# Performance work log

Hardware: AMD Instinct MI355X
Metric: run time of the kernel (lower is better)

Reference implementation:

```python
import jax, jax.numpy as jnp
import numpy as np

B, N, D = 2, 2048, 1024
H, FD, HD = 16, 16, 64
ENC = 512
EPS = 1e-12
RD = 4.0            # sqrt(scale_dim=feature_dim=16)
RRD = 2.0           # sqrt(RD)
R2 = float(np.sqrt(2.0))


def taylor_exp(x):
    # x: [..., fd] -> [..., 1 + fd + fd*fd]
    x2 = (x[..., :, None] * x[..., None, :]).reshape(*x.shape[:-1], FD * FD) / R2
    return jnp.concatenate([jnp.ones_like(x[..., :1]), x / RRD, x2 / RD], axis=-1)


def setup_inputs() -> dict:
    key = jax.random.key(0)
    ks = jax.random.split(key, 7)
    s = 1.0 / np.sqrt(D)
    x = jax.random.normal(ks[0], (B, N, D), dtype=jnp.float32)
    Wq = jax.random.normal(ks[1], (H * FD, D), dtype=jnp.float32) * s
    Wk = jax.random.normal(ks[2], (H * FD, D), dtype=jnp.float32) * s
    Wv = jax.random.normal(ks[3], (H * HD, D), dtype=jnp.float32) * s
    Wk_enc = jax.random.normal(ks[4], (H * FD, D), dtype=jnp.float32) * s
    Wv_enc = jax.random.normal(ks[5], (H * HD, D), dtype=jnp.float32) * s
    Wout = jax.random.normal(ks[6], (D, H * HD), dtype=jnp.float32) * s
    return {"x": x, "Wq": Wq, "Wk": Wk, "Wv": Wv,
            "Wk_enc": Wk_enc, "Wv_enc": Wv_enc, "Wout": Wout}


def reference(x, Wq, Wk, Wv, Wk_enc, Wv_enc, Wout):
    b, n, _ = x.shape
    # projections -> [b, h, n, *]
    q = (x @ Wq.T).reshape(b, n, H, FD).transpose(0, 2, 1, 3)
    k = (x @ Wk.T).reshape(b, n, H, FD).transpose(0, 2, 1, 3)
    v = (x @ Wv.T).reshape(b, n, H, HD).transpose(0, 2, 1, 3)
    # encoder prefix
    x_enc = x[:, :ENC]
    k_enc = (x_enc @ Wk_enc.T).reshape(b, ENC, H, FD).transpose(0, 2, 1, 3)
    v_enc = (x_enc @ Wv_enc.T).reshape(b, ENC, H, HD).transpose(0, 2, 1, 3)
    # Taylor feature maps: fd -> 1 + fd + fd^2 = 273
    k_enc_f = taylor_exp(k_enc)
    q_f = taylor_exp(q)
    k_f = taylor_exp(k)
    # causal decoder attention (unnormalized)
    A_qk = jnp.einsum('bhnd,bhmd->bhnm', q_f, k_f)
    A_qk = jnp.tril(A_qk)
    y1 = jnp.einsum('bhnm,bhme->bhne', A_qk, v)
    # cross attention to encoder prefix
    A_qk2 = jnp.einsum('bhnd,bhmd->bhnm', q_f, k_enc_f)
    y2 = jnp.einsum('bhnm,bhme->bhne', A_qk2, v_enc)
    # shared normalizer: enc sum + causal cumsum of decoder key features
    k_state = k_enc_f.sum(axis=2, keepdims=True) + jnp.cumsum(k_f, axis=2)
    z = 1.0 / ((q_f * k_state).sum(axis=-1) + EPS)  # [b, h, n]
    out = (y1 + y2) * z[..., None]                  # [b, h, n, hd]
    out = out.transpose(0, 2, 1, 3).reshape(b, n, H * HD)
    return out @ Wout.T
```

## Files before the change

kernel.cpp:

```cpp
#include <hip/hip_runtime.h>

#define B_    2
#define N_    2048
#define H_    16
#define HD_   64
#define ENC_  512
#define FP_   288
#define CHK_  64
#define NC_   32
#define SSZ_  18720
#define C2C_  0.17677669529663687f
#define EPS_  1e-12f

using s8v   = __attribute__((ext_vector_type(8))) short;
using s4v   = __attribute__((ext_vector_type(4))) short;
using h8v   = __attribute__((ext_vector_type(8))) _Float16;
using f4v   = __attribute__((ext_vector_type(4))) float;
using u16x4 = __attribute__((ext_vector_type(4))) unsigned short;
typedef unsigned short ushort_t;

__device__ __forceinline__ unsigned short f16q(float x) {
    _Float16 h = (_Float16)x;
    return __builtin_bit_cast(unsigned short, h);
}
__device__ __forceinline__ float f16f(unsigned short u) {
    return (float)__builtin_bit_cast(_Float16, u);
}
__device__ __forceinline__ u16x4 f16q4(float4 v) {
    return (u16x4){f16q(v.x), f16q(v.y), f16q(v.z), f16q(v.w)};
}

#define MFMAH_ __builtin_amdgcn_mfma_f32_16x16x32_f16

__device__ __forceinline__ void gld16(const void* g, void* l) {
    __builtin_amdgcn_global_load_lds(
        (const __attribute__((address_space(1))) unsigned int*)g,
        (__attribute__((address_space(3))) unsigned int*)l, 16, 0, 0);
}

__device__ __forceinline__ int xcd_swz(int b, int nwg) {
    int q = nwg >> 3, r = nwg & 7;
    int xcd = b & 7, loc = b >> 3;
    return (xcd < r ? xcd * (q + 1) : r * (q + 1) + (xcd - r) * q) + loc;
}

#define X_F4   1048576
#define W1_F4  393216
#define W2_F4  327680
#define WO_F4  262144

__global__ __launch_bounds__(256) void split_all(
    const float* __restrict__ x,
    const float* __restrict__ Wq, const float* __restrict__ Wk,
    const float* __restrict__ Wv, const float* __restrict__ Wke,
    const float* __restrict__ Wve, const float* __restrict__ Wout,
    ushort_t* __restrict__ xh,
    ushort_t* __restrict__ w1, ushort_t* __restrict__ w2,
    ushort_t* __restrict__ wo)
{
    int gid = blockIdx.x * 256 + threadIdx.x;
    if (gid < X_F4) {
        ((u16x4*)xh)[gid] = f16q4(((const float4*)x)[gid]);
    } else if (gid < X_F4 + W1_F4) {
        int i = gid - X_F4;
        int row = i >> 8, c4 = i & 255;
        const float* s = (row < 256) ? Wq + (size_t)row * 1024
                       : (row < 512) ? Wk + (size_t)(row - 256) * 1024
                                     : Wv + (size_t)(row - 512) * 1024;
        ((u16x4*)w1)[i] = f16q4(*(const float4*)(s + c4 * 4));
    } else if (gid < X_F4 + W1_F4 + W2_F4) {
        int i = gid - X_F4 - W1_F4;
        int row = i >> 8, c4 = i & 255;
        const float* s = (row < 256) ? Wke + (size_t)row * 1024
                                     : Wve + (size_t)(row - 256) * 1024;
        ((u16x4*)w2)[i] = f16q4(*(const float4*)(s + c4 * 4));
    } else {
        int i = gid - X_F4 - W1_F4 - W2_F4;
        ((u16x4*)wo)[i] = f16q4(((const float4*)Wout)[i]);
    }
}

template <int SHIFT>
__device__ __forceinline__ void bg128(
    const ushort_t* __restrict__ Ah, const ushort_t* __restrict__ Wh,
    int bx, int by, int rowjump,
    ushort_t* SM, f4v (&acc)[4][4])
{
    int t = threadIdx.x;
    int w = t >> 6, lane = t & 63;
    int row0 = by * 128, col0 = bx * 128;
    int wrow = (w >> 1) * 64, wcol = (w & 1) * 64;
    int fr = lane & 15, g = lane >> 4;

    int c0 = lane, c1 = 64 + lane;
    int r0 = w * 32 + (c0 >> 2), k80 = (c0 & 3) * 8;
    int r1 = w * 32 + (c1 >> 2), k81 = (c1 & 3) * 8;
    int gr0 = row0 + r0, gr1 = row0 + r1;
    size_t a0 = (size_t)(gr0 >> SHIFT) * rowjump + (gr0 & ((1 << SHIFT) - 1));
    size_t a1 = (size_t)(gr1 >> SHIFT) * rowjump + (gr1 & ((1 << SHIFT) - 1));
    const ushort_t* pA0 = Ah + a0 * 1024 + k80;
    const ushort_t* pA1 = Ah + a1 * 1024 + k81;
    const ushort_t* pW0 = Wh + (size_t)(col0 + r0) * 1024 + k80;
    const ushort_t* pW1 = Wh + (size_t)(col0 + r1) * 1024 + k81;
    int woff = w * 1024;

    #pragma unroll
    for (int mt = 0; mt < 4; ++mt)
        #pragma unroll
        for (int nt = 0; nt < 4; ++nt) acc[mt][nt] = (f4v){0.f, 0.f, 0.f, 0.f};

    auto STAGE = [&](int buf, int k0) {
        ushort_t* Bp = SM + buf * 8192;
        gld16(pA0 + k0, Bp + woff);
        gld16(pA1 + k0, Bp + woff + 512);
        gld16(pW0 + k0, Bp + 4096 + woff);
        gld16(pW1 + k0, Bp + 4096 + woff + 512);
    };

    STAGE(0, 0);
    __syncthreads();
    int cur = 0;
    for (int k0 = 0; k0 < 1024; k0 += 32) {
        if (k0 + 32 < 1024) STAGE(cur ^ 1, k0 + 32);
        ushort_t* Bp = SM + cur * 8192;
        h8v a_h[4], b_[4];
        #pragma unroll
        for (int mt = 0; mt < 4; ++mt)
            a_h[mt] = *(const h8v*)&Bp[(wrow + mt * 16 + fr) * 32 + g * 8];
        #pragma unroll
        for (int nt = 0; nt < 4; ++nt)
            b_[nt] = *(const h8v*)&Bp[4096 + (wcol + nt * 16 + fr) * 32 + g * 8];
        #pragma unroll
        for (int mt = 0; mt < 4; ++mt)
            #pragma unroll
            for (int nt = 0; nt < 4; ++nt)
                acc[mt][nt] = MFMAH_(a_h[mt], b_[nt], acc[mt][nt], 0, 0, 0);
        __syncthreads();
        cur ^= 1;
    }
}

__global__ __launch_bounds__(256) void proj2(
    const ushort_t* __restrict__ xh,
    const ushort_t* __restrict__ w1, const ushort_t* __restrict__ w2,
    ushort_t* __restrict__ tmpq, ushort_t* __restrict__ tmpk, ushort_t* __restrict__ v,
    ushort_t* __restrict__ tmpke, ushort_t* __restrict__ ve)
{
    __shared__ ushort_t SM[16384];
    f4v acc[4][4];
    int blk = xcd_swz(blockIdx.x, 464);
    int t = threadIdx.x, w = t >> 6, lane = t & 63;
    int wrow = (w >> 1) * 64, wcol = (w & 1) * 64;
    int fr = lane & 15, g = lane >> 4;

    if (blk < 384) {
        int bx = blk % 12, by = blk / 12;
        bg128<12>(xh, w1, bx, by, 0, SM, acc);
        int row0 = by * 128, col0 = bx * 128;
        #pragma unroll
        for (int mt = 0; mt < 4; ++mt)
            #pragma unroll
            for (int nt = 0; nt < 4; ++nt)
                #pragma unroll
                for (int r4 = 0; r4 < 4; ++r4) {
                    int r  = row0 + wrow + mt * 16 + g * 4 + r4;
                    int cc = col0 + wcol + nt * 16 + fr;
                    ushort_t val = f16q(acc[mt][nt][r4]);
                    if (cc < 256)      tmpq[(size_t)r * 256 + cc] = val;
                    else if (cc < 512) tmpk[(size_t)r * 256 + (cc - 256)] = val;
                    else {
                        int c2 = cc - 512, hh = c2 >> 6, jj = c2 & 63;
                        int bb = r >> 11, n = r & 2047;
                        v[(((size_t)(bb * 16 + hh)) * 2048 + n) * 64 + jj] = val;
                    }
                }
    } else {
        int r2 = blk - 384;
        int bx = r2 % 10, by = r2 / 10;
        bg128<9>(xh, w2, bx, by, 2048, SM, acc);
        int row0 = by * 128, col0 = bx * 128;
        #pragma unroll
        for (int mt = 0; mt < 4; ++mt)
            #pragma unroll
            for (int nt = 0; nt < 4; ++nt)
                #pragma unroll
                for (int r4 = 0; r4 < 4; ++r4) {
                    int r  = row0 + wrow + mt * 16 + g * 4 + r4;
                    int cc = col0 + wcol + nt * 16 + fr;
                    ushort_t val = f16q(acc[mt][nt][r4]);
                    if (cc < 256) tmpke[(size_t)r * 256 + cc] = val;
                    else {
                        int c2 = cc - 256, hh = c2 >> 6, jj = c2 & 63;
                        int bb = r >> 9, n = r & 511;
                        ve[(((size_t)(bb * 16 + hh)) * 512 + n) * 64 + jj] = val;
                    }
                }
    }
}

__global__ __launch_bounds__(256) void out_gemm(
    const ushort_t* __restrict__ Atn, const ushort_t* __restrict__ Wh,
    float* __restrict__ out)
{
    __shared__ ushort_t SM[16384];
    f4v acc[4][4];
    int blk = xcd_swz(blockIdx.x, 256);
    int bx = blk & 7, by = blk >> 3;
    bg128<12>(Atn, Wh, bx, by, 0, SM, acc);
    int t = threadIdx.x, w = t >> 6, lane = t & 63;
    int wrow = (w >> 1) * 64, wcol = (w & 1) * 64;
    int fr = lane & 15, g = lane >> 4;
    int row0 = by * 128, col0 = bx * 128;
    #pragma unroll
    for (int mt = 0; mt < 4; ++mt)
        #pragma unroll
        for (int nt = 0; nt < 4; ++nt)
            #pragma unroll
            for (int r4 = 0; r4 < 4; ++r4) {
                int r  = row0 + wrow + mt * 16 + g * 4 + r4;
                int cc = col0 + wcol + nt * 16 + fr;
                out[(size_t)r * 1024 + cc] = acc[mt][nt][r4];
            }
}

__device__ __forceinline__ void st_stage(
    const ushort_t* __restrict__ Kp, const ushort_t* __restrict__ V,
    size_t krow0, size_t vrow0, int h, int t,
    float* ksT, ushort_t* VTH)
{
    {
        int r = t >> 2, q4 = t & 3;
        s4v kv = *(const s4v*)&Kp[(krow0 + r) * 256 + h * 16 + q4 * 4];
        ksT[(q4 * 4 + 0) * 68 + r] = f16f((ushort_t)kv[0]);
        ksT[(q4 * 4 + 1) * 68 + r] = f16f((ushort_t)kv[1]);
        ksT[(q4 * 4 + 2) * 68 + r] = f16f((ushort_t)kv[2]);
        ksT[(q4 * 4 + 3) * 68 + r] = f16f((ushort_t)kv[3]);
    }
    if (t < 64) ksT[16 * 68 + t] = 1.0f;
    {
        int r = t & 63, jg = t >> 6;
        const ushort_t* vrow = &V[(vrow0 + r) * HD_ + jg * 16];
        s8v v0 = *(const s8v*)(vrow);
        s8v v1 = *(const s8v*)(vrow + 8);
        int j0 = jg * 16;
        #pragma unroll
        for (int e = 0; e < 8; ++e) VTH[(j0 + e) * 72 + r] = (ushort_t)v0[e];
        #pragma unroll
        for (int e = 0; e < 8; ++e) VTH[(j0 + 8 + e) * 72 + r] = (ushort_t)v1[e];
    }
    if (t < 64) VTH[64 * 72 + t] = 0x3C00;
}

__device__ __forceinline__ void st_ftile(
    const float* ksT, int ft, int fr, int g,
    const h8v (&AHf)[2][5], f4v (&acc)[5])
{
    int f = ft * 16 + fr;
    int fi, fj; float scale;
    if (f == 0)       { fi = 16; fj = 16; scale = 1.0f; }
    else if (f < 17)  { fi = f - 1; fj = 16; scale = 0.5f; }
    else if (f < 273) { fi = (f - 17) >> 4; fj = (f - 17) & 15; scale = C2C_; }
    else              { fi = 16; fj = 16; scale = 0.0f; }
    #pragma unroll
    for (int ks2 = 0; ks2 < 2; ++ks2) {
        const float* pa = ksT + fi * 68 + ks2 * 32 + g * 8;
        const float* pb = ksT + fj * 68 + ks2 * 32 + g * 8;
        h8v bv;
        #pragma unroll
        for (int e = 0; e < 8; ++e) bv[e] = (_Float16)(pa[e] * pb[e] * scale);
        #pragma unroll
        for (int jt = 0; jt < 5; ++jt)
            acc[jt] = MFMAH_(AHf[ks2][jt], bv, acc[jt], 0, 0, 0);
    }
}

__global__ __launch_bounds__(256) void state_all(
    const ushort_t* __restrict__ Kpe, const ushort_t* __restrict__ Ve, ushort_t* __restrict__ Se,
    const ushort_t* __restrict__ Kpc, const ushort_t* __restrict__ Vc, ushort_t* __restrict__ Sc)
{
    __shared__ float ksT[17 * 68];
    __shared__ ushort_t VTH[80 * 72];
    int blk = blockIdx.x, t = threadIdx.x;
    int w = t >> 6, lane = t & 63, fr = lane & 15, g = lane >> 4;

    for (int i = t; i < 15 * 72; i += 256) VTH[65 * 72 + i] = 0;

    if (blk >= 160) {
        int b2 = blk - 160;
        int c = b2 & 31, bh = b2 >> 5;
        int b = bh >> 4, h = bh & 15;
        ushort_t* Sg = Sc + ((size_t)bh * NC_ + c) * SSZ_;
        st_stage(Kpc, Vc, (size_t)b * 2048 + c * 64, (size_t)bh * 2048 + c * 64,
                 h, t, ksT, VTH);
        __syncthreads();
        h8v AHf[2][5];
        #pragma unroll
        for (int ks2 = 0; ks2 < 2; ++ks2)
            #pragma unroll
            for (int jt = 0; jt < 5; ++jt)
                AHf[ks2][jt] = *(const h8v*)&VTH[(jt * 16 + fr) * 72 + ks2 * 32 + g * 8];
        for (int ft = w; ft < 18; ft += 4) {
            f4v acc[5];
            #pragma unroll
            for (int jt = 0; jt < 5; ++jt) acc[jt] = (f4v){0.f, 0.f, 0.f, 0.f};
            st_ftile(ksT, ft, fr, g, AHf, acc);
            #pragma unroll
            for (int jt = 0; jt < 5; ++jt)
                #pragma unroll
                for (int r4 = 0; r4 < 4; ++r4) {
                    int j = jt * 16 + g * 4 + r4;
                    if (j < 65) Sg[(size_t)j * FP_ + ft * 16 + fr] = f16q(acc[jt][r4]);
                }
        }
    } else {
        int bh = blk / 5, fg = blk % 5;
        int b = bh >> 4, h = bh & 15;
        int ft = fg * 4 + w;
        ushort_t* Sg = Se + (size_t)bh * SSZ_;
        f4v acc[5];
        #pragma unroll
        for (int jt = 0; jt < 5; ++jt) acc[jt] = (f4v){0.f, 0.f, 0.f, 0.f};
        for (int m0 = 0; m0 < 512; m0 += 64) {
            if (m0) __syncthreads();
            st_stage(Kpe, Ve, (size_t)b * 512 + m0, (size_t)bh * 512 + m0,
                     h, t, ksT, VTH);
            __syncthreads();
            if (ft < 18) {
                h8v AHf[2][5];
                #pragma unroll
                for (int ks2 = 0; ks2 < 2; ++ks2)
                    #pragma unroll
                    for (int jt = 0; jt < 5; ++jt)
                        AHf[ks2][jt] = *(const h8v*)&VTH[(jt * 16 + fr) * 72 + ks2 * 32 + g * 8];
                st_ftile(ksT, ft, fr, g, AHf, acc);
            }
        }
        if (ft < 18) {
            #pragma unroll
            for (int jt = 0; jt < 5; ++jt)
                #pragma unroll
                for (int r4 = 0; r4 < 4; ++r4) {
                    int j = jt * 16 + g * 4 + r4;
                    if (j < 65) Sg[(size_t)j * FP_ + ft * 16 + fr] = f16q(acc[jt][r4]);
                }
        }
    }
}

__global__ __launch_bounds__(256) void prefix_scan(
    ushort_t* __restrict__ Sloc, const ushort_t* __restrict__ Senc)
{
    const int Q = SSZ_ / 4;
    int gid = blockIdx.x * 256 + threadIdx.x;
    if (gid >= 32 * Q) return;
    int bh = gid / Q, e = gid - bh * Q;
    s4v ev = *(const s4v*)(Senc + (size_t)bh * SSZ_ + e * 4);
    float run[4];
    #pragma unroll
    for (int u = 0; u < 4; ++u) run[u] = f16f((ushort_t)ev[u]);
    ushort_t* Sb = Sloc + (size_t)bh * NC_ * SSZ_ + e * 4;
    s4v tv[NC_];
    #pragma unroll
    for (int c2 = 0; c2 < NC_; ++c2)
        tv[c2] = *(const s4v*)(Sb + (size_t)c2 * SSZ_);
    #pragma unroll
    for (int c2 = 0; c2 < NC_; ++c2) {
        s4v o;
        #pragma unroll
        for (int u = 0; u < 4; ++u) {
            o[u] = (short)f16q(run[u]);
            run[u] += f16f((ushort_t)tv[c2][u]);
        }
        *(s4v*)(Sb + (size_t)c2 * SSZ_) = o;
    }
}

template<int FW>
__device__ __forceinline__ void y2_issue(
    const ushort_t* __restrict__ Sth, int f0, int t, s8v& r0, s8v& r1, s8v& r2)
{
    constexpr int NS = FW / 8;
    constexpr int TOT = 65 * NS;
    int s1 = t + 256, s2 = t + 512;
    r0 = *(const s8v*)(Sth + (size_t)(t / NS) * FP_ + f0 + (t % NS) * 8);
    if (s1 < TOT) r1 = *(const s8v*)(Sth + (size_t)(s1 / NS) * FP_ + f0 + (s1 % NS) * 8);
    if (FW == 64 && s2 < TOT) r2 = *(const s8v*)(Sth + (size_t)(s2 / NS) * FP_ + f0 + (s2 % NS) * 8);
}

template<int FW>
__device__ __forceinline__ void y2_write(
    ushort_t* STH, int t, const s8v& r0, const s8v& r1, const s8v& r2)
{
    constexpr int NS = FW / 8;
    constexpr int TOT = 65 * NS;
    int s1 = t + 256, s2 = t + 512;
    *(s8v*)&STH[(t / NS) * 72 + (t % NS) * 8] = r0;
    if (s1 < TOT) *(s8v*)&STH[(s1 / NS) * 72 + (s1 % NS) * 8] = r1;
    if (FW == 64 && s2 < TOT) *(s8v*)&STH[(s2 / NS) * 72 + (s2 % NS) * 8] = r2;
}

template<int FW>
__device__ __forceinline__ void qf_gen(int f0, const float* qs, ushort_t* QF1, int t)
{
    for (int i = t; i < 64 * FW; i += 256) {
        int row = i / FW, cc = i % FW;
        int f = f0 + cc;
        float qv;
        if (f == 0)       qv = 1.0f;
        else if (f < 17)  qv = qs[row * 20 + (f - 1)] * 0.5f;
        else if (f < 273) qv = qs[row * 20 + ((f - 17) >> 4)] * qs[row * 20 + ((f - 17) & 15)] * C2C_;
        else              qv = 0.0f;
        QF1[row * 72 + cc] = f16q(qv);
    }
}

template<int FW>
__device__ __forceinline__ void y2_mfma(
    const ushort_t* QF1, const ushort_t* STH,
    f4v (&acc)[5], int w, int fr, int g)
{
    #pragma unroll
    for (int ks2 = 0; ks2 < FW / 32; ++ks2) {
        h8v a = *(const h8v*)&QF1[(16 * w + fr) * 72 + ks2 * 32 + g * 8];
        #pragma unroll
        for (int jt = 0; jt < 5; ++jt) {
            h8v b = *(const h8v*)&STH[(jt * 16 + fr) * 72 + ks2 * 32 + g * 8];
            acc[jt] = MFMAH_(a, b, acc[jt], 0, 0, 0);
        }
    }
}

__global__ __launch_bounds__(256) void attn_chunk(
    const ushort_t* __restrict__ qp, const ushort_t* __restrict__ kp,
    const ushort_t* __restrict__ v, const ushort_t* __restrict__ Spre,
    ushort_t* __restrict__ atn)
{
    __shared__ ushort_t U[14976];
    __shared__ float qs[64 * 20];
    __shared__ float den_s[64];
    ushort_t* AH  = U;
    ushort_t* QH  = U + 9216;
    ushort_t* KH  = U + 11776;
    ushort_t* VTH = U + 9216;
    ushort_t* QF1 = U;
    ushort_t* STH = U + 9216;

    int bid = blockIdx.x;
    int bh = bid >> 5, c = bid & 31;
    int b = bh >> 4, h = bh & 15;
    int t = threadIdx.x;
    int w = t >> 6, lane = t & 63, fr = lane & 15, g = lane >> 4;
    int rowbase = b * N_ + c * CHK_;
    const ushort_t* Sth = Spre + ((size_t)bh * NC_ + c) * SSZ_;

    int rqk = t >> 2, q4 = t & 3;
    s4v qv = *(const s4v*)&qp[(size_t)(rowbase + rqk) * 256 + h * 16 + q4 * 4];
    s4v kv = *(const s4v*)&kp[(size_t)(rowbase + rqk) * 256 + h * 16 + q4 * 4];
    s8v rA0 = {}, rA1 = {}, rA2 = {};
    y2_issue<64>(Sth, 0, t, rA0, rA1, rA2);
    int mv = t & 63, jg0 = t >> 6;
    const ushort_t* vr = &v[((size_t)bh * N_ + c * CHK_ + mv) * HD_ + jg0 * 16];
    s8v rv0 = *(const s8v*)(vr);
    s8v rv1 = *(const s8v*)(vr + 8);

    {
        *(s4v*)&QH[rqk * 40 + q4 * 4] = qv;
        *(s4v*)&KH[rqk * 40 + q4 * 4] = kv;
        s4v z4 = (s4v){0, 0, 0, 0};
        *(s4v*)&QH[rqk * 40 + 16 + q4 * 4] = z4;
        *(s4v*)&KH[rqk * 40 + 16 + q4 * 4] = z4;
        qs[rqk * 20 + q4 * 4 + 0] = f16f((ushort_t)qv[0]);
        qs[rqk * 20 + q4 * 4 + 1] = f16f((ushort_t)qv[1]);
        qs[rqk * 20 + q4 * 4 + 2] = f16f((ushort_t)qv[2]);
        qs[rqk * 20 + q4 * 4 + 3] = f16f((ushort_t)qv[3]);
    }
    __syncthreads();

    {
        h8v qh = *(const h8v*)&QH[(16 * w + fr) * 40 + g * 8];
        f4v sacc[4];
        #pragma unroll
        for (int jt = 0; jt < 4; ++jt) sacc[jt] = (f4v){0.f, 0.f, 0.f, 0.f};
        #pragma unroll
        for (int jt = 0; jt < 4; ++jt) {
            h8v kh = *(const h8v*)&KH[(jt * 16 + fr) * 40 + g * 8];
            sacc[jt] = MFMAH_(qh, kh, sacc[jt], 0, 0, 0);
        }
        __syncthreads();
        #pragma unroll
        for (int jt = 0; jt < 4; ++jt)
            #pragma unroll
            for (int r4 = 0; r4 < 4; ++r4) {
                int row = 16 * w + g * 4 + r4, col = jt * 16 + fr;
                float s = sacc[jt][r4];
                float a = (row >= col) ? (fmaf(s, 0.25f, 1.0f) + s * s * 0.03125f) : 0.f;
                AH[row * 72 + col] = f16q(a);
            }
    }
    {
        int j0 = jg0 * 16;
        #pragma unroll
        for (int e = 0; e < 8; ++e) VTH[(j0 + e) * 72 + mv] = (ushort_t)rv0[e];
        #pragma unroll
        for (int e = 0; e < 8; ++e) VTH[(j0 + 8 + e) * 72 + mv] = (ushort_t)rv1[e];
    }
    if (t < 64) VTH[64 * 72 + t] = 0x3C00;
    for (int i = t; i < 15 * 72; i += 256) VTH[65 * 72 + i] = 0;
    __syncthreads();

    f4v acc[5];
    #pragma unroll
    for (int jt = 0; jt < 5; ++jt) acc[jt] = (f4v){0.f, 0.f, 0.f, 0.f};
    #pragma unroll
    for (int ks2 = 0; ks2 < 2; ++ks2) {
        h8v ah = *(const h8v*)&AH[(16 * w + fr) * 72 + ks2 * 32 + g * 8];
        #pragma unroll
        for (int jt = 0; jt < 5; ++jt) {
            h8v b = *(const h8v*)&VTH[(jt * 16 + fr) * 72 + ks2 * 32 + g * 8];
            acc[jt] = MFMAH_(ah, b, acc[jt], 0, 0, 0);
        }
    }
    __syncthreads();

    #pragma unroll
    for (int p = 0; p < 4; ++p) {
        y2_write<64>(STH, t, rA0, rA1, rA2);
        if (p < 3) y2_issue<64>(Sth, (p + 1) * 64, t, rA0, rA1, rA2);
        else       y2_issue<32>(Sth, 256,          t, rA0, rA1, rA2);
        qf_gen<64>(p * 64, qs, QF1, t);
        __syncthreads();
        y2_mfma<64>(QF1, STH, acc, w, fr, g);
        __syncthreads();
    }
    y2_write<32>(STH, t, rA0, rA1, rA2);
    qf_gen<32>(256, qs, QF1, t);
    __syncthreads();
    y2_mfma<32>(QF1, STH, acc, w, fr, g);

    if (fr == 0) {
        #pragma unroll
        for (int r4 = 0; r4 < 4; ++r4)
            den_s[16 * w + g * 4 + r4] = acc[4][r4];
    }
    __syncthreads();
    #pragma unroll
    for (int r4 = 0; r4 < 4; ++r4) {
        float z = 1.0f / (den_s[16 * w + g * 4 + r4] + EPS_);
        int row = rowbase + 16 * w + g * 4 + r4;
        #pragma unroll
        for (int jt = 0; jt < 4; ++jt) {
            float val = acc[jt][r4] * z;
            atn[(size_t)row * 1024 + h * 64 + jt * 16 + fr] = f16q(val);
        }
    }
}

extern "C" void kernel_launch(void* const* d_in, const int* in_sizes, int n_in,
                              void* d_out, int out_size, void* d_ws, size_t ws_size,
                              hipStream_t stream)
{
    const float* x    = (const float*)d_in[0];
    const float* Wq   = (const float*)d_in[1];
    const float* Wk   = (const float*)d_in[2];
    const float* Wv   = (const float*)d_in[3];
    const float* Wke  = (const float*)d_in[4];
    const float* Wve  = (const float*)d_in[5];
    const float* Wout = (const float*)d_in[6];
    float* out = (float*)d_out;

    ushort_t* usws  = (ushort_t*)d_ws;
    ushort_t* tmpq  = usws;
    ushort_t* tmpk  = tmpq  + (size_t)1048576;
    ushort_t* tmpke = tmpk  + (size_t)1048576;
    ushort_t* v     = tmpke + (size_t)262144;
    ushort_t* ve    = v     + (size_t)4194304;
    ushort_t* Sloc  = ve    + (size_t)1048576;
    ushort_t* Senc  = Sloc  + (size_t)19169280;
    ushort_t* xh    = Senc  + (size_t)599040;
    ushort_t* wo    = xh    + (size_t)4194304;
    ushort_t* w1 = Sloc;
    ushort_t* w2 = w1 + (size_t)1572864;
    ushort_t* atn = xh;

    dim3 blk(256);

    split_all<<<7936, blk, 0, stream>>>(x, Wq, Wk, Wv, Wke, Wve, Wout,
                                        xh, w1, w2, wo);
    proj2<<<464, blk, 0, stream>>>(xh, w1, w2, tmpq, tmpk, v, tmpke, ve);
    state_all<<<160 + 32 * NC_, blk, 0, stream>>>(tmpke, ve, Senc, tmpk, v, Sloc);
    prefix_scan<<<585, blk, 0, stream>>>(Sloc, Senc);
    attn_chunk<<<32 * NC_, blk, 0, stream>>>(tmpq, tmpk, v, Sloc, atn);
    out_gemm<<<256, blk, 0, stream>>>(atn, wo, out);
}
```

Measured before the change: 103.5 us.

## Fuse chunk state computation with prefix scan in one sequential kernel

Replaces the parallel per-chunk state kernel and the separate prefix-scan kernel with one kernel. Each block walks the encoder rows and then all decoder chunks for one (batch, head, feature group), keeping the running state in registers and writing exclusive prefixes directly. It prefetches the next unit's K/V into registers while computing the current one. This removes a launch and the extra global read/write pass of the scan, at the cost of far fewer blocks (160) and a long serial chain per block.

```diff
diff --git a/kernel.cpp b/kernel.cpp
--- a/kernel.cpp
+++ b/kernel.cpp
@@ -223,155 +223,102 @@
             }
 }
 
-__device__ __forceinline__ void st_stage(
-    const ushort_t* __restrict__ Kp, const ushort_t* __restrict__ V,
-    size_t krow0, size_t vrow0, int h, int t,
-    float* ksT, ushort_t* VTH)
-{
-    {
-        int r = t >> 2, q4 = t & 3;
-        s4v kv = *(const s4v*)&Kp[(krow0 + r) * 256 + h * 16 + q4 * 4];
-        ksT[(q4 * 4 + 0) * 68 + r] = f16f((ushort_t)kv[0]);
-        ksT[(q4 * 4 + 1) * 68 + r] = f16f((ushort_t)kv[1]);
-        ksT[(q4 * 4 + 2) * 68 + r] = f16f((ushort_t)kv[2]);
-        ksT[(q4 * 4 + 3) * 68 + r] = f16f((ushort_t)kv[3]);
-    }
-    if (t < 64) ksT[16 * 68 + t] = 1.0f;
-    {
-        int r = t & 63, jg = t >> 6;
-        const ushort_t* vrow = &V[(vrow0 + r) * HD_ + jg * 16];
-        s8v v0 = *(const s8v*)(vrow);
-        s8v v1 = *(const s8v*)(vrow + 8);
-        int j0 = jg * 16;
-        #pragma unroll
-        for (int e = 0; e < 8; ++e) VTH[(j0 + e) * 72 + r] = (ushort_t)v0[e];
-        #pragma unroll
-        for (int e = 0; e < 8; ++e) VTH[(j0 + 8 + e) * 72 + r] = (ushort_t)v1[e];
-    }
-    if (t < 64) VTH[64 * 72 + t] = 0x3C00;
-}
-
-__device__ __forceinline__ void st_ftile(
-    const float* ksT, int ft, int fr, int g,
-    const h8v (&AHf)[2][5], f4v (&acc)[5])
-{
+__global__ __launch_bounds__(256) void state_prefix(
+    const ushort_t* __restrict__ kpe, const ushort_t* __restrict__ ve,
+    const ushort_t* __restrict__ kpc, const ushort_t* __restrict__ vc,
+    ushort_t* __restrict__ Spre)
+{
+    __shared__ float ksT[17 * 68];
+    __shared__ ushort_t VTH[80 * 72];
+    int blk = blockIdx.x;
+    int fg = blk % 5, bh = blk / 5;
+    int b = bh >> 4, h = bh & 15;
+    int t = threadIdx.x;
+    int w = t >> 6, lane = t & 63, fr = lane & 15, g = lane >> 4;
+    int ft = fg * 4 + w;
+    bool fvalid = ft < 18;
+
     int f = ft * 16 + fr;
     int fi, fj; float scale;
     if (f == 0)       { fi = 16; fj = 16; scale = 1.0f; }
     else if (f < 17)  { fi = f - 1; fj = 16; scale = 0.5f; }
     else if (f < 273) { fi = (f - 17) >> 4; fj = (f - 17) & 15; scale = C2C_; }
     else              { fi = 16; fj = 16; scale = 0.0f; }
-    #pragma unroll
-    for (int ks2 = 0; ks2 < 2; ++ks2) {
-        const float* pa = ksT + fi * 68 + ks2 * 32 + g * 8;
-        const float* pb = ksT + fj * 68 + ks2 * 32 + g * 8;
-        h8v bv;
-        #pragma unroll
-        for (int e = 0; e < 8; ++e) bv[e] = (_Float16)(pa[e] * pb[e] * scale);
-        #pragma unroll
-        for (int jt = 0; jt < 5; ++jt)
-            acc[jt] = MFMAH_(AHf[ks2][jt], bv, acc[jt], 0, 0, 0);
-    }
-}
-
-__global__ __launch_bounds__(256) void state_all(
-    const ushort_t* __restrict__ Kpe, const ushort_t* __restrict__ Ve, ushort_t* __restrict__ Se,
-    const ushort_t* __restrict__ Kpc, const ushort_t* __restrict__ Vc, ushort_t* __restrict__ Sc)
-{
-    __shared__ float ksT[17 * 68];
-    __shared__ ushort_t VTH[80 * 72];
-    int blk = blockIdx.x, t = threadIdx.x;
-    int w = t >> 6, lane = t & 63, fr = lane & 15, g = lane >> 4;
 
     for (int i = t; i < 15 * 72; i += 256) VTH[65 * 72 + i] = 0;
 
-    if (blk >= 160) {
-        int b2 = blk - 160;
-        int c = b2 & 31, bh = b2 >> 5;
-        int b = bh >> 4, h = bh & 15;
-        ushort_t* Sg = Sc + ((size_t)bh * NC_ + c) * SSZ_;
-        st_stage(Kpc, Vc, (size_t)b * 2048 + c * 64, (size_t)bh * 2048 + c * 64,
-                 h, t, ksT, VTH);
-        __syncthreads();
-        h8v AHf[2][5];
-        #pragma unroll
-        for (int ks2 = 0; ks2 < 2; ++ks2)
-            #pragma unroll
-            for (int jt = 0; jt < 5; ++jt)
-                AHf[ks2][jt] = *(const h8v*)&VTH[(jt * 16 + fr) * 72 + ks2 * 32 + g * 8];
-        for (int ft = w; ft < 18; ft += 4) {
-            f4v acc[5];
-            #pragma unroll
-            for (int jt = 0; jt < 5; ++jt) acc[jt] = (f4v){0.f, 0.f, 0.f, 0.f};
-            st_ftile(ksT, ft, fr, g, AHf, acc);
+    int rk_r = t >> 2, rk_q4 = t & 3;
+    int mv = t & 63, jg = t >> 6, j0 = jg * 16;
+
+    auto ld_unit = [&](int u, s4v& rk, s8v& rv0, s8v& rv1) {
+        if (u < 8) {
+            rk = *(const s4v*)&kpe[((size_t)b * 512 + u * 64 + rk_r) * 256 + h * 16 + rk_q4 * 4];
+            const ushort_t* vr = &ve[((size_t)bh * 512 + u * 64 + mv) * HD_ + j0];
+            rv0 = *(const s8v*)vr; rv1 = *(const s8v*)(vr + 8);
+        } else {
+            int c = u - 8;
+            rk = *(const s4v*)&kpc[((size_t)b * 2048 + c * 64 + rk_r) * 256 + h * 16 + rk_q4 * 4];
+            const ushort_t* vr = &vc[((size_t)bh * 2048 + c * 64 + mv) * HD_ + j0];
+            rv0 = *(const s8v*)vr; rv1 = *(const s8v*)(vr + 8);
+        }
+    };
+    auto wr_unit = [&](const s4v& rk, const s8v& rv0, const s8v& rv1) {
+        ksT[(rk_q4 * 4 + 0) * 68 + rk_r] = f16f((ushort_t)rk[0]);
+        ksT[(rk_q4 * 4 + 1) * 68 + rk_r] = f16f((ushort_t)rk[1]);
+        ksT[(rk_q4 * 4 + 2) * 68 + rk_r] = f16f((ushort_t)rk[2]);
+        ksT[(rk_q4 * 4 + 3) * 68 + rk_r] = f16f((ushort_t)rk[3]);
+        if (t < 64) ksT[16 * 68 + t] = 1.0f;
+        #pragma unroll
+        for (int e = 0; e < 8; ++e) VTH[(j0 + e) * 72 + mv] = (ushort_t)rv0[e];
+        #pragma unroll
+        for (int e = 0; e < 8; ++e) VTH[(j0 + 8 + e) * 72 + mv] = (ushort_t)rv1[e];
+        if (t < 64) VTH[64 * 72 + t] = 0x3C00;
+    };
+
+    f4v run[5];
+    #pragma unroll
+    for (int jt = 0; jt < 5; ++jt) run[jt] = (f4v){0.f, 0.f, 0.f, 0.f};
+
+    s4v rk; s8v rv0, rv1;
+    ld_unit(0, rk, rv0, rv1);
+    wr_unit(rk, rv0, rv1);
+    __syncthreads();
+
+    for (int u = 0; u < 40; ++u) {
+        s4v nk; s8v nv0, nv1;
+        if (u < 39) ld_unit(u + 1, nk, nv0, nv1);
+
+        if (u >= 8 && fvalid) {
+            ushort_t* Sg = Spre + ((size_t)bh * NC_ + (u - 8)) * SSZ_;
             #pragma unroll
             for (int jt = 0; jt < 5; ++jt)
                 #pragma unroll
                 for (int r4 = 0; r4 < 4; ++r4) {
                     int j = jt * 16 + g * 4 + r4;
-                    if (j < 65) Sg[(size_t)j * FP_ + ft * 16 + fr] = f16q(acc[jt][r4]);
+                    if (j < 65) Sg[(size_t)j * FP_ + f] = f16q(run[jt][r4]);
                 }
         }
-    } else {
-        int bh = blk / 5, fg = blk % 5;
-        int b = bh >> 4, h = bh & 15;
-        int ft = fg * 4 + w;
-        ushort_t* Sg = Se + (size_t)bh * SSZ_;
-        f4v acc[5];
-        #pragma unroll
-        for (int jt = 0; jt < 5; ++jt) acc[jt] = (f4v){0.f, 0.f, 0.f, 0.f};
-        for (int m0 = 0; m0 < 512; m0 += 64) {
-            if (m0) __syncthreads();
-            st_stage(Kpe, Ve, (size_t)b * 512 + m0, (size_t)bh * 512 + m0,
-                     h, t, ksT, VTH);
+
+        if (fvalid) {
+            #pragma unroll
+            for (int ks2 = 0; ks2 < 2; ++ks2) {
+                const float* pa = ksT + fi * 68 + ks2 * 32 + g * 8;
+                const float* pb = ksT + fj * 68 + ks2 * 32 + g * 8;
+                h8v bv;
+                #pragma unroll
+                for (int e = 0; e < 8; ++e) bv[e] = (_Float16)(pa[e] * pb[e] * scale);
+                #pragma unroll
+                for (int jt = 0; jt < 5; ++jt) {
+                    h8v av = *(const h8v*)&VTH[(jt * 16 + fr) * 72 + ks2 * 32 + g * 8];
+                    run[jt] = MFMAH_(av, bv, run[jt], 0, 0, 0);
+                }
+            }
+        }
+        __syncthreads();
+        if (u < 39) {
+            wr_unit(nk, nv0, nv1);
             __syncthreads();
-            if (ft < 18) {
-                h8v AHf[2][5];
-                #pragma unroll
-                for (int ks2 = 0; ks2 < 2; ++ks2)
-                    #pragma unroll
-                    for (int jt = 0; jt < 5; ++jt)
-                        AHf[ks2][jt] = *(const h8v*)&VTH[(jt * 16 + fr) * 72 + ks2 * 32 + g * 8];
-                st_ftile(ksT, ft, fr, g, AHf, acc);
-            }
-        }
-        if (ft < 18) {
-            #pragma unroll
-            for (int jt = 0; jt < 5; ++jt)
-                #pragma unroll
-                for (int r4 = 0; r4 < 4; ++r4) {
-                    int j = jt * 16 + g * 4 + r4;
-                    if (j < 65) Sg[(size_t)j * FP_ + ft * 16 + fr] = f16q(acc[jt][r4]);
-                }
-        }
-    }
-}
-
-__global__ __launch_bounds__(256) void prefix_scan(
-    ushort_t* __restrict__ Sloc, const ushort_t* __restrict__ Senc)
-{
-    const int Q = SSZ_ / 4;
-    int gid = blockIdx.x * 256 + threadIdx.x;
-    if (gid >= 32 * Q) return;
-    int bh = gid / Q, e = gid - bh * Q;
-    s4v ev = *(const s4v*)(Senc + (size_t)bh * SSZ_ + e * 4);
-    float run[4];
-    #pragma unroll
-    for (int u = 0; u < 4; ++u) run[u] = f16f((ushort_t)ev[u]);
-    ushort_t* Sb = Sloc + (size_t)bh * NC_ * SSZ_ + e * 4;
-    s4v tv[NC_];
-    #pragma unroll
-    for (int c2 = 0; c2 < NC_; ++c2)
-        tv[c2] = *(const s4v*)(Sb + (size_t)c2 * SSZ_);
-    #pragma unroll
-    for (int c2 = 0; c2 < NC_; ++c2) {
-        s4v o;
-        #pragma unroll
-        for (int u = 0; u < 4; ++u) {
-            o[u] = (short)f16q(run[u]);
-            run[u] += f16f((ushort_t)tv[c2][u]);
-        }
-        *(s4v*)(Sb + (size_t)c2 * SSZ_) = o;
+        }
     }
 }
 
@@ -575,8 +522,7 @@
     ushort_t* v     = tmpke + (size_t)262144;
     ushort_t* ve    = v     + (size_t)4194304;
     ushort_t* Sloc  = ve    + (size_t)1048576;
-    ushort_t* Senc  = Sloc  + (size_t)19169280;
-    ushort_t* xh    = Senc  + (size_t)599040;
+    ushort_t* xh    = Sloc  + (size_t)19169280;
     ushort_t* wo    = xh    + (size_t)4194304;
     ushort_t* w1 = Sloc;
     ushort_t* w2 = w1 + (size_t)1572864;
@@ -587,8 +533,7 @@
     split_all<<<7936, blk, 0, stream>>>(x, Wq, Wk, Wv, Wke, Wve, Wout,
                                         xh, w1, w2, wo);
     proj2<<<464, blk, 0, stream>>>(xh, w1, w2, tmpq, tmpk, v, tmpke, ve);
-    state_all<<<160 + 32 * NC_, blk, 0, stream>>>(tmpke, ve, Senc, tmpk, v, Sloc);
-    prefix_scan<<<585, blk, 0, stream>>>(Sloc, Senc);
+    state_prefix<<<160, blk, 0, stream>>>(tmpke, ve, tmpk, v, Sloc);
     attn_chunk<<<32 * NC_, blk, 0, stream>>>(tmpq, tmpk, v, Sloc, atn);
     out_gemm<<<256, blk, 0, stream>>>(atn, wo, out);
 }
```

After: 121.1 us. 1.17x slower.
